# Kernel optimization log

Measured on AMD Instinct MI355X. Metric: run time of the kernel, lower is better.

Reference implementation:

```python
import jax, jax.numpy as jnp
import numpy as np

N_EMBD = 1024
N_HEAD = 16

def setup_inputs() -> dict:
    key = jax.random.key(0)
    ks = jax.random.split(key, 5)
    B, T, C = 4, 2048, N_EMBD
    s = 0.02
    return {
        'x': jax.random.normal(ks[0], (B, T, C), jnp.float32),
        'w_attn': jax.random.normal(ks[1], (C, 3 * C), jnp.float32) * s,
        'b_attn': jax.random.normal(ks[2], (3 * C,), jnp.float32) * s,
        'w_proj': jax.random.normal(ks[3], (C, C), jnp.float32) * s,
        'b_proj': jax.random.normal(ks[4], (C,), jnp.float32) * s,
    }

def reference(x, w_attn, b_attn, w_proj, b_proj):
    B, T, C = x.shape
    H = N_HEAD
    D = C // H  # head dim
    qkv = x @ w_attn + b_attn                      # [B,T,3C]
    q, k, v = jnp.split(qkv, 3, axis=-1)
    q = q.reshape(B, T, H, D).transpose(0, 2, 1, 3)  # [B,H,T,D]
    k = k.reshape(B, T, H, D).transpose(0, 2, 1, 3)
    v = v.reshape(B, T, H, D).transpose(0, 2, 1, 3)
    att = jnp.einsum('bhqd,bhkd->bhqk', q, k) * (1.0 / jnp.sqrt(jnp.float32(D)))
    causal = jnp.tril(jnp.ones((T, T), bool))
    att = jnp.where(causal[None, None], att, jnp.float32(-jnp.inf))
    att = jax.nn.softmax(att, axis=-1)
    y = jnp.einsum('bhqk,bhkd->bhqd', att, v)      # [B,H,T,D]
    y = y.transpose(0, 2, 1, 3).reshape(B, T, C)
    return y @ w_proj + b_proj
```

## Files before the change

### kernel.cpp

```cpp
#include <hip/hip_runtime.h>
#include <math.h>

typedef short s16x8 __attribute__((ext_vector_type(8)));
typedef unsigned short u16;
typedef unsigned short u16x4 __attribute__((ext_vector_type(4)));
typedef float f32x4 __attribute__((ext_vector_type(4)));

__device__ __forceinline__ f32x4 mfma16(s16x8 a, s16x8 b, f32x4 c) {
  return __builtin_amdgcn_mfma_f32_16x16x32_bf16(a, b, c, 0, 0, 0);
}

__device__ __forceinline__ u16 f2bf(float f) {
  unsigned u = __builtin_bit_cast(unsigned, f);
  u = (u + 0x7fffu + ((u >> 16) & 1u)) >> 16;
  return (u16)u;
}

__device__ __forceinline__ unsigned pk_trunc(float hi, float lo) {
  return __builtin_amdgcn_perm(__builtin_bit_cast(unsigned, hi),
                               __builtin_bit_cast(unsigned, lo), 0x07060302u);
}

__device__ __forceinline__ void gll16(const void* g, void* l) {
  __builtin_amdgcn_global_load_lds((__attribute__((address_space(1))) void*)(void*)g,
                                   (__attribute__((address_space(3))) void*)l,
                                   16, 0, 0);
}

__device__ __forceinline__ void lds_fence() {
  asm volatile("s_waitcnt lgkmcnt(0)" ::: "memory");
}

__global__ __launch_bounds__(256) void k_convert_x(const float* __restrict__ x,
                                                   u16* __restrict__ xb) {
  int i = (blockIdx.x * 256 + threadIdx.x) * 8;
  const float4* xv = (const float4*)(x + i);
  float4 a = xv[0], b = xv[1];
  union { s16x8 v; u16 s[8]; } r;
  r.s[0] = f2bf(a.x); r.s[1] = f2bf(a.y); r.s[2] = f2bf(a.z); r.s[3] = f2bf(a.w);
  r.s[4] = f2bf(b.x); r.s[5] = f2bf(b.y); r.s[6] = f2bf(b.z); r.s[7] = f2bf(b.w);
  *(s16x8*)(xb + i) = r.v;
}

__global__ __launch_bounds__(256) void k_transpose_w(const float* __restrict__ in,
                                                     u16* __restrict__ out, int R, int C) {
  __shared__ float tile[32][33];
  int c0 = blockIdx.x * 32, r0 = blockIdx.y * 32;
  int tx = threadIdx.x & 31, ty = threadIdx.x >> 5;
#pragma unroll
  for (int s = 0; s < 4; ++s)
    tile[ty + 8 * s][tx] = in[(size_t)(r0 + ty + 8 * s) * C + c0 + tx];
  __syncthreads();
#pragma unroll
  for (int s = 0; s < 4; ++s)
    out[(size_t)(c0 + ty + 8 * s) * R + r0 + tx] = f2bf(tile[tx][ty + 8 * s]);
}

template <int EPI>
__global__ __launch_bounds__(256) void k_gemm(const u16* __restrict__ A,
                                              const u16* __restrict__ Bt,
                                              const float* __restrict__ bias,
                                              float* __restrict__ outp,
                                              u16* __restrict__ q_out,
                                              u16* __restrict__ k_out,
                                              u16* __restrict__ vt_out,
                                              int K, int nIter) {
  __shared__ u16 As[2][4096];
  __shared__ u16 Bs[2][4096];
  int tid = threadIdx.x, w = tid >> 6, l = tid & 63;
  int r = l & 15, qd = l >> 4;
  int id = blockIdx.x;
  int xcd = id & 7, s0 = id >> 3;
  int mBlk = xcd * 8 + (s0 & 7);
  int nBlk = s0 >> 3;
  f32x4 acc[4][4] = {};

  const u16* ga[2]; const u16* gb[2]; int lgrp[2];
#pragma unroll
  for (int qq = 0; qq < 2; ++qq) {
    int grp = 2 * w + qq;
    int rowA = mBlk * 128 + grp * 16 + (l >> 2);
    int rowB = nBlk * 128 + grp * 16 + (l >> 2);
    int kcol = (l & 3) * 8;
    ga[qq] = A + (size_t)rowA * K + kcol;
    gb[qq] = Bt + (size_t)rowB * K + kcol;
    lgrp[qq] = grp * 512;
  }
  int aoff = ((w & 1) * 4) * 512 + r * 32 + qd * 8;
  int boff = ((w >> 1) * 4) * 512 + r * 32 + qd * 8;

  auto stageg = [&](int kt, int buf) {
#pragma unroll
    for (int qq = 0; qq < 2; ++qq) {
      gll16(ga[qq] + kt * 32, As[buf] + lgrp[qq]);
      gll16(gb[qq] + kt * 32, Bs[buf] + lgrp[qq]);
    }
  };

  stageg(0, 0);
  __syncthreads();

  for (int kt = 0; kt < nIter; ++kt) {
    int cur = kt & 1;
    if (kt + 1 < nIter) stageg(kt + 1, cur ^ 1);
    s16x8 af[4], bf[4];
#pragma unroll
    for (int i = 0; i < 4; ++i) af[i] = *(const s16x8*)(As[cur] + aoff + i * 512);
#pragma unroll
    for (int j = 0; j < 4; ++j) bf[j] = *(const s16x8*)(Bs[cur] + boff + j * 512);
#pragma unroll
    for (int i = 0; i < 4; ++i)
#pragma unroll
      for (int j = 0; j < 4; ++j) acc[i][j] = mfma16(af[i], bf[j], acc[i][j]);
    __syncthreads();
  }

  const float QSCALE = 0.125f * 1.44269504088896f;
  int rowBase = mBlk * 128 + (w & 1) * 64;
  int colBase = nBlk * 128 + (w >> 1) * 64;
#pragma unroll
  for (int i = 0; i < 4; ++i) {
#pragma unroll
    for (int j = 0; j < 4; ++j) {
      int col = colBase + j * 16 + r;
      float bv = bias[col];
      float vv[4];
#pragma unroll
      for (int g = 0; g < 4; ++g) vv[g] = acc[i][j][g] + bv;
      int row0 = rowBase + i * 16 + qd * 4;
      if (EPI == 0) {
        int which = col >> 10;
        int rem = col & 1023;
        int hh = rem >> 6, dd = rem & 63;
        int bb = row0 >> 11, tt0 = row0 & 2047;
        if (which == 2) {
          u16x4 pk;
#pragma unroll
          for (int g = 0; g < 4; ++g) pk[g] = f2bf(vv[g]);
          *(u16x4*)(vt_out + (((size_t)(bb * 16 + hh)) * 64 + dd) * 2048 + tt0) = pk;
        } else {
          u16* base = (which == 0) ? q_out : k_out;
#pragma unroll
          for (int g = 0; g < 4; ++g) {
            float v = vv[g];
            if (which == 0) v *= QSCALE;
            base[(((size_t)(bb * 16 + hh)) * 2048 + tt0 + g) * 64 + dd] = f2bf(v);
          }
        }
      } else {
#pragma unroll
        for (int g = 0; g < 4; ++g)
          outp[(size_t)(row0 + g) * 1024 + col] = vv[g];
      }
    }
  }
}

__global__ __launch_bounds__(256, 2) void k_attn(const u16* __restrict__ qg,
                                                 const u16* __restrict__ kg,
                                                 const u16* __restrict__ vtg,
                                                 u16* __restrict__ yg) {
  __shared__ u16 Ks[3][64 * 64];
  __shared__ u16 Vs[3][64 * 64];
  __shared__ u16 Ps[4][64 * 64];

  int id = blockIdx.x;
  int xcd = id & 7;
  int slot = id >> 3;
  int bx = slot & 7;
  int bh = ((slot >> 3) << 3) | xcd;
  int bb = bh >> 4, hh = bh & 15;
  int tid = threadIdx.x, w = tid >> 6, l = tid & 63;
  int r = l & 15, qd = l >> 4;
  int psw = (r & 7) * 8;

  const int chunk[4] = {bx, 15 - bx, 16 + bx, 31 - bx};
  const int nend[4]  = {bx + 1, 16 - bx, 17 + bx, 32 - bx};
  int nmax = 32 - bx;
  int qloc = w * 16 + r;

  s16x8 qf[4][2];
#pragma unroll
  for (int c = 0; c < 4; ++c) {
    int qbase = chunk[c] * 64 + w * 16;
#pragma unroll
    for (int s = 0; s < 2; ++s)
      qf[c][s] = *(const s16x8*)(qg + ((size_t)bh * 2048 + qbase + r) * 64 + s * 32 + qd * 8);
  }

  s16x8 onesf;
#pragma unroll
  for (int e = 0; e < 8; ++e) onesf[e] = (short)0x3F80;

  f32x4 o[4][4] = {};
  f32x4 lacc[4] = {};

  int rl = l >> 3;
  int cg = (l & 7) ^ rl;
  const u16* kbase = kg + (size_t)bh * 2048 * 64;
  const u16* vbase = vtg + (size_t)bh * 64 * 2048;

  auto stage = [&](int kt, int buf) {
    int kk0 = kt * 64;
#pragma unroll
    for (int p = 0; p < 2; ++p) {
      int row = p * 32 + w * 8 + rl;
      gll16(kbase + ((size_t)(kk0 + row)) * 64 + cg * 8, Ks[buf] + p * 2048 + w * 512);
      gll16(vbase + (size_t)row * 2048 + kk0 + cg * 8, Vs[buf] + p * 2048 + w * 512);
    }
  };

  auto qk_smax = [&](int kt, int buf) {
    f32x4 sacc[4][4];
#pragma unroll
    for (int c = 0; c < 4; ++c)
      if (kt < nend[c])
#pragma unroll
        for (int j = 0; j < 4; ++j) sacc[c][j] = f32x4{0.f, 0.f, 0.f, 0.f};
    __builtin_amdgcn_s_setprio(1);
#pragma unroll
    for (int s = 0; s < 2; ++s) {
#pragma unroll
      for (int j = 0; j < 4; ++j) {
        s16x8 kf = *(const s16x8*)(Ks[buf] + (16 * j + r) * 64 + ((s * 4 + qd) ^ (r & 7)) * 8);
#pragma unroll
        for (int c = 0; c < 4; ++c)
          if (kt < nend[c]) sacc[c][j] = mfma16(kf, qf[c][s], sacc[c][j]);
      }
    }
    __builtin_amdgcn_s_setprio(0);
#pragma unroll
    for (int c = 0; c < 4; ++c) {
      if (kt >= nend[c]) continue;
      bool needMask = (kt == chunk[c]);
#pragma unroll
      for (int j = 0; j < 4; ++j) {
        float p0, p1, p2, p3;
        if (needMask) {
          int kb0 = 16 * j + 4 * qd;
          p0 = (kb0 + 0 > qloc) ? 0.f : __builtin_amdgcn_exp2f(sacc[c][j][0]);
          p1 = (kb0 + 1 > qloc) ? 0.f : __builtin_amdgcn_exp2f(sacc[c][j][1]);
          p2 = (kb0 + 2 > qloc) ? 0.f : __builtin_amdgcn_exp2f(sacc[c][j][2]);
          p3 = (kb0 + 3 > qloc) ? 0.f : __builtin_amdgcn_exp2f(sacc[c][j][3]);
        } else {
          p0 = __builtin_amdgcn_exp2f(sacc[c][j][0]);
          p1 = __builtin_amdgcn_exp2f(sacc[c][j][1]);
          p2 = __builtin_amdgcn_exp2f(sacc[c][j][2]);
          p3 = __builtin_amdgcn_exp2f(sacc[c][j][3]);
        }
        uint2 pk;
        pk.x = pk_trunc(p1, p0);
        pk.y = pk_trunc(p3, p2);
        *(uint2*)(Ps[w] + (c * 16 + r) * 64 + ((j * 16 + qd * 4) ^ psw)) = pk;
      }
    }
  };

  auto pv = [&](int kt, int buf) {
    __builtin_amdgcn_s_setprio(1);
#pragma unroll
    for (int s = 0; s < 2; ++s) {
      s16x8 pa[4];
#pragma unroll
      for (int c = 0; c < 4; ++c)
        if (kt < nend[c]) {
          pa[c] = *(const s16x8*)(Ps[w] + (c * 16 + r) * 64 + ((s * 32 + qd * 8) ^ psw));
          lacc[c] = mfma16(onesf, pa[c], lacc[c]);
        }
#pragma unroll
      for (int j = 0; j < 4; ++j) {
        s16x8 vf = *(const s16x8*)(Vs[buf] + (16 * j + r) * 64 + ((s * 4 + qd) ^ (r & 7)) * 8);
#pragma unroll
        for (int c = 0; c < 4; ++c)
          if (kt < nend[c]) o[c][j] = mfma16(vf, pa[c], o[c][j]);
      }
    }
    __builtin_amdgcn_s_setprio(0);
  };

  stage(0, 0);
  stage(1, 1);
  __syncthreads();
  qk_smax(0, 0);
  lds_fence();

  int b0 = 0, b1 = 1, b2 = 2;
  for (int kt = 0; kt < nmax; ++kt) {
    if (kt + 2 < nmax) stage(kt + 2, b2);
    pv(kt, b0);
    if (kt + 1 < nmax) qk_smax(kt + 1, b1);
    __syncthreads();
    int t = b0; b0 = b1; b1 = b2; b2 = t;
  }

#pragma unroll
  for (int c = 0; c < 4; ++c) {
    int qbase = chunk[c] * 64 + w * 16;
    float inv = 1.0f / lacc[c][0];
    size_t rowoff = ((size_t)bb * 2048 + qbase + r) * 1024 + hh * 64;
#pragma unroll
    for (int j = 0; j < 4; ++j) {
      u16x4 yv;
      yv[0] = f2bf(o[c][j][0] * inv);
      yv[1] = f2bf(o[c][j][1] * inv);
      yv[2] = f2bf(o[c][j][2] * inv);
      yv[3] = f2bf(o[c][j][3] * inv);
      *(u16x4*)(yg + rowoff + 16 * j + 4 * qd) = yv;
    }
  }
}

extern "C" void kernel_launch(void* const* d_in, const int* in_sizes, int n_in,
                              void* d_out, int out_size, void* d_ws, size_t ws_size,
                              hipStream_t stream) {
  const float* x      = (const float*)d_in[0];
  const float* w_attn = (const float*)d_in[1];
  const float* b_attn = (const float*)d_in[2];
  const float* w_proj = (const float*)d_in[3];
  const float* b_proj = (const float*)d_in[4];
  float* out = (float*)d_out;

  char* ws = (char*)d_ws;
  size_t off = 0;
  auto alloc = [&](size_t bytes) -> void* {
    void* p = ws + off;
    off += (bytes + 255) & ~(size_t)255;
    return p;
  };
  const size_t BT = 8192, C = 1024;
  u16* xb  = (u16*)alloc(BT * C * 2);
  u16* waT = (u16*)alloc(3072 * 1024 * 2);
  u16* wpT = (u16*)alloc(1024 * 1024 * 2);
  u16* qb  = (u16*)alloc(BT * C * 2);
  u16* kb  = (u16*)alloc(BT * C * 2);
  u16* vtb = (u16*)alloc(BT * C * 2);
  (void)ws_size; (void)in_sizes; (void)n_in; (void)out_size;

  k_convert_x<<<4096, 256, 0, stream>>>(x, xb);
  k_transpose_w<<<dim3(96, 32), 256, 0, stream>>>(w_attn, waT, 1024, 3072);
  k_transpose_w<<<dim3(32, 32), 256, 0, stream>>>(w_proj, wpT, 1024, 1024);
  k_gemm<0><<<1536, 256, 0, stream>>>(xb, waT, b_attn, nullptr, qb, kb, vtb, 1024, 32);
  k_attn<<<512, 256, 0, stream>>>(qb, kb, vtb, xb );
  k_gemm<1><<<512, 256, 0, stream>>>(xb, wpT, b_proj, out, nullptr, nullptr, nullptr, 1024, 32);
}
```

Baseline: 264.0 us.

## Keep P in registers via permlane swaps, halve chunks per block, double grid

The attention kernel now gives each block 2 balanced query chunks instead of 4 and launches twice as many blocks. It replaces the LDS round-trip for the softmax probabilities P with in-register v_permlane32/16 swaps that rearrange the QK accumulator layout into the PV operand layout. It also drops the three-stage software pipeline for a simpler double-buffered loop. The smaller LDS footprint and the change to __launch_bounds__(256,4) are meant to raise occupancy and cut LDS traffic, at the cost of losing QK/PV overlap across iterations and reloading K/V tiles twice as often.

```diff
diff --git a/kernel.cpp b/kernel.cpp
--- a/kernel.cpp
+++ b/kernel.cpp
@@ -21,14 +21,16 @@
                                __builtin_bit_cast(unsigned, lo), 0x07060302u);
 }
 
+__device__ __forceinline__ s16x8 mk_pa(unsigned a, unsigned b, unsigned c, unsigned d) {
+  union { unsigned u[4]; s16x8 h; } t;
+  t.u[0] = a; t.u[1] = b; t.u[2] = c; t.u[3] = d;
+  return t.h;
+}
+
 __device__ __forceinline__ void gll16(const void* g, void* l) {
   __builtin_amdgcn_global_load_lds((__attribute__((address_space(1))) void*)(void*)g,
                                    (__attribute__((address_space(3))) void*)l,
                                    16, 0, 0);
-}
-
-__device__ __forceinline__ void lds_fence() {
-  asm volatile("s_waitcnt lgkmcnt(0)" ::: "memory");
 }
 
 __global__ __launch_bounds__(256) void k_convert_x(const float* __restrict__ x,
@@ -156,33 +158,30 @@
   }
 }
 
-__global__ __launch_bounds__(256, 2) void k_attn(const u16* __restrict__ qg,
+__global__ __launch_bounds__(256, 4) void k_attn(const u16* __restrict__ qg,
                                                  const u16* __restrict__ kg,
                                                  const u16* __restrict__ vtg,
                                                  u16* __restrict__ yg) {
-  __shared__ u16 Ks[3][64 * 64];
-  __shared__ u16 Vs[3][64 * 64];
-  __shared__ u16 Ps[4][64 * 64];
+  __shared__ u16 Ks[2][64 * 64];
+  __shared__ u16 Vs[2][64 * 64];
 
   int id = blockIdx.x;
   int xcd = id & 7;
   int slot = id >> 3;
-  int bx = slot & 7;
-  int bh = ((slot >> 3) << 3) | xcd;
+  int bx = slot & 15;
+  int bh = ((slot >> 4) << 3) | xcd;
   int bb = bh >> 4, hh = bh & 15;
   int tid = threadIdx.x, w = tid >> 6, l = tid & 63;
   int r = l & 15, qd = l >> 4;
-  int psw = (r & 7) * 8;
-
-  const int chunk[4] = {bx, 15 - bx, 16 + bx, 31 - bx};
-  const int nend[4]  = {bx + 1, 16 - bx, 17 + bx, 32 - bx};
+
+  const int chunk0 = bx, chunk1 = 31 - bx;
   int nmax = 32 - bx;
   int qloc = w * 16 + r;
 
-  s16x8 qf[4][2];
-#pragma unroll
-  for (int c = 0; c < 4; ++c) {
-    int qbase = chunk[c] * 64 + w * 16;
+  s16x8 qf[2][2];
+#pragma unroll
+  for (int c = 0; c < 2; ++c) {
+    int qbase = (c ? chunk1 : chunk0) * 64 + w * 16;
 #pragma unroll
     for (int s = 0; s < 2; ++s)
       qf[c][s] = *(const s16x8*)(qg + ((size_t)bh * 2048 + qbase + r) * 64 + s * 32 + qd * 8);
@@ -192,8 +191,8 @@
 #pragma unroll
   for (int e = 0; e < 8; ++e) onesf[e] = (short)0x3F80;
 
-  f32x4 o[4][4] = {};
-  f32x4 lacc[4] = {};
+  f32x4 o[2][4] = {};
+  f32x4 lacc[2] = {};
 
   int rl = l >> 3;
   int cg = (l & 7) ^ rl;
@@ -210,92 +209,92 @@
     }
   };
 
-  auto qk_smax = [&](int kt, int buf) {
-    f32x4 sacc[4][4];
-#pragma unroll
-    for (int c = 0; c < 4; ++c)
-      if (kt < nend[c])
-#pragma unroll
-        for (int j = 0; j < 4; ++j) sacc[c][j] = f32x4{0.f, 0.f, 0.f, 0.f};
+  auto smax = [&](f32x4 (&sc)[4], s16x8 (&pac)[2], bool mask) {
+    unsigned pk[4][2];
+#pragma unroll
+    for (int j = 0; j < 4; ++j) {
+      float p0, p1, p2, p3;
+      if (mask) {
+        int kb0 = 16 * j + 4 * qd;
+        p0 = (kb0 + 0 > qloc) ? 0.f : __builtin_amdgcn_exp2f(sc[j][0]);
+        p1 = (kb0 + 1 > qloc) ? 0.f : __builtin_amdgcn_exp2f(sc[j][1]);
+        p2 = (kb0 + 2 > qloc) ? 0.f : __builtin_amdgcn_exp2f(sc[j][2]);
+        p3 = (kb0 + 3 > qloc) ? 0.f : __builtin_amdgcn_exp2f(sc[j][3]);
+      } else {
+        p0 = __builtin_amdgcn_exp2f(sc[j][0]);
+        p1 = __builtin_amdgcn_exp2f(sc[j][1]);
+        p2 = __builtin_amdgcn_exp2f(sc[j][2]);
+        p3 = __builtin_amdgcn_exp2f(sc[j][3]);
+      }
+      pk[j][0] = pk_trunc(p1, p0);
+      pk[j][1] = pk_trunc(p3, p2);
+    }
+#pragma unroll
+    for (int s = 0; s < 2; ++s) {
+      unsigned a0 = pk[2 * s][0], b0 = pk[2 * s + 1][0];
+      asm("v_permlane32_swap_b32 %0, %1" : "+v"(a0), "+v"(b0));
+      asm("v_permlane16_swap_b32 %0, %1" : "+v"(a0), "+v"(b0));
+      unsigned a1 = pk[2 * s][1], b1 = pk[2 * s + 1][1];
+      asm("v_permlane32_swap_b32 %0, %1" : "+v"(a1), "+v"(b1));
+      asm("v_permlane16_swap_b32 %0, %1" : "+v"(a1), "+v"(b1));
+      pac[s] = mk_pa(a0, a1, b0, b1);
+    }
+  };
+
+  stage(0, 0);
+  __syncthreads();
+
+  for (int kt = 0; kt < nmax; ++kt) {
+    int cur = kt & 1;
+    if (kt + 1 < nmax) stage(kt + 1, cur ^ 1);
+    bool act0 = (kt <= bx);
+
+    f32x4 s0[4], s1[4];
+#pragma unroll
+    for (int j = 0; j < 4; ++j) {
+      s1[j] = f32x4{0.f, 0.f, 0.f, 0.f};
+      if (act0) s0[j] = f32x4{0.f, 0.f, 0.f, 0.f};
+    }
     __builtin_amdgcn_s_setprio(1);
 #pragma unroll
     for (int s = 0; s < 2; ++s) {
 #pragma unroll
       for (int j = 0; j < 4; ++j) {
-        s16x8 kf = *(const s16x8*)(Ks[buf] + (16 * j + r) * 64 + ((s * 4 + qd) ^ (r & 7)) * 8);
-#pragma unroll
-        for (int c = 0; c < 4; ++c)
-          if (kt < nend[c]) sacc[c][j] = mfma16(kf, qf[c][s], sacc[c][j]);
+        s16x8 kf = *(const s16x8*)(Ks[cur] + (16 * j + r) * 64 + ((s * 4 + qd) ^ (r & 7)) * 8);
+        s1[j] = mfma16(kf, qf[1][s], s1[j]);
+        if (act0) s0[j] = mfma16(kf, qf[0][s], s0[j]);
       }
     }
     __builtin_amdgcn_s_setprio(0);
-#pragma unroll
-    for (int c = 0; c < 4; ++c) {
-      if (kt >= nend[c]) continue;
-      bool needMask = (kt == chunk[c]);
+
+    s16x8 pa0[2], pa1[2];
+    smax(s1, pa1, kt == chunk1);
+    lacc[1] = mfma16(onesf, pa1[0], lacc[1]);
+    lacc[1] = mfma16(onesf, pa1[1], lacc[1]);
+    if (act0) {
+      smax(s0, pa0, kt == chunk0);
+      lacc[0] = mfma16(onesf, pa0[0], lacc[0]);
+      lacc[0] = mfma16(onesf, pa0[1], lacc[0]);
+    }
+
+    __builtin_amdgcn_s_setprio(1);
+#pragma unroll
+    for (int s = 0; s < 2; ++s) {
 #pragma unroll
       for (int j = 0; j < 4; ++j) {
-        float p0, p1, p2, p3;
-        if (needMask) {
-          int kb0 = 16 * j + 4 * qd;
-          p0 = (kb0 + 0 > qloc) ? 0.f : __builtin_amdgcn_exp2f(sacc[c][j][0]);
-          p1 = (kb0 + 1 > qloc) ? 0.f : __builtin_amdgcn_exp2f(sacc[c][j][1]);
-          p2 = (kb0 + 2 > qloc) ? 0.f : __builtin_amdgcn_exp2f(sacc[c][j][2]);
-          p3 = (kb0 + 3 > qloc) ? 0.f : __builtin_amdgcn_exp2f(sacc[c][j][3]);
-        } else {
-          p0 = __builtin_amdgcn_exp2f(sacc[c][j][0]);
-          p1 = __builtin_amdgcn_exp2f(sacc[c][j][1]);
-          p2 = __builtin_amdgcn_exp2f(sacc[c][j][2]);
-          p3 = __builtin_amdgcn_exp2f(sacc[c][j][3]);
-        }
-        uint2 pk;
-        pk.x = pk_trunc(p1, p0);
-        pk.y = pk_trunc(p3, p2);
-        *(uint2*)(Ps[w] + (c * 16 + r) * 64 + ((j * 16 + qd * 4) ^ psw)) = pk;
+        s16x8 vf = *(const s16x8*)(Vs[cur] + (16 * j + r) * 64 + ((s * 4 + qd) ^ (r & 7)) * 8);
+        o[1][j] = mfma16(vf, pa1[s], o[1][j]);
+        if (act0) o[0][j] = mfma16(vf, pa0[s], o[0][j]);
       }
     }
-  };
-
-  auto pv = [&](int kt, int buf) {
-    __builtin_amdgcn_s_setprio(1);
-#pragma unroll
-    for (int s = 0; s < 2; ++s) {
-      s16x8 pa[4];
-#pragma unroll
-      for (int c = 0; c < 4; ++c)
-        if (kt < nend[c]) {
-          pa[c] = *(const s16x8*)(Ps[w] + (c * 16 + r) * 64 + ((s * 32 + qd * 8) ^ psw));
-          lacc[c] = mfma16(onesf, pa[c], lacc[c]);
-        }
-#pragma unroll
-      for (int j = 0; j < 4; ++j) {
-        s16x8 vf = *(const s16x8*)(Vs[buf] + (16 * j + r) * 64 + ((s * 4 + qd) ^ (r & 7)) * 8);
-#pragma unroll
-        for (int c = 0; c < 4; ++c)
-          if (kt < nend[c]) o[c][j] = mfma16(vf, pa[c], o[c][j]);
-      }
-    }
     __builtin_amdgcn_s_setprio(0);
-  };
-
-  stage(0, 0);
-  stage(1, 1);
-  __syncthreads();
-  qk_smax(0, 0);
-  lds_fence();
-
-  int b0 = 0, b1 = 1, b2 = 2;
-  for (int kt = 0; kt < nmax; ++kt) {
-    if (kt + 2 < nmax) stage(kt + 2, b2);
-    pv(kt, b0);
-    if (kt + 1 < nmax) qk_smax(kt + 1, b1);
+
     __syncthreads();
-    int t = b0; b0 = b1; b1 = b2; b2 = t;
-  }
-
-#pragma unroll
-  for (int c = 0; c < 4; ++c) {
-    int qbase = chunk[c] * 64 + w * 16;
+  }
+
+#pragma unroll
+  for (int c = 0; c < 2; ++c) {
+    int qbase = (c ? chunk1 : chunk0) * 64 + w * 16;
     float inv = 1.0f / lacc[c][0];
     size_t rowoff = ((size_t)bb * 2048 + qbase + r) * 1024 + hh * 64;
 #pragma unroll
@@ -340,6 +339,6 @@
   k_transpose_w<<<dim3(96, 32), 256, 0, stream>>>(w_attn, waT, 1024, 3072);
   k_transpose_w<<<dim3(32, 32), 256, 0, stream>>>(w_proj, wpT, 1024, 1024);
   k_gemm<0><<<1536, 256, 0, stream>>>(xb, waT, b_attn, nullptr, qb, kb, vtb, 1024, 32);
-  k_attn<<<512, 256, 0, stream>>>(qb, kb, vtb, xb );
+  k_attn<<<1024, 256, 0, stream>>>(qb, kb, vtb, xb );
   k_gemm<1><<<512, 256, 0, stream>>>(xb, wpT, b_proj, out, nullptr, nullptr, nullptr, 1024, 32);
 }
```

Result: faster. 245.2 us (-7.1%).
